# Kernel tuning notes

Measured on AMD Instinct MI355X. Metric: run time of the kernel, lower is better.

Reference implementation:

```python
import jax, jax.numpy as jnp
import numpy as np

OBS_DIM, ACT_DIM, LATENT_DIM, BELIEF_DIM, T = 128, 32, 512, 1024, 32768


def setup_inputs() -> dict:
    key = jax.random.key(0)
    ks = jax.random.split(key, 8)
    s_ih = 1.0 / np.sqrt(BELIEF_DIM)
    s_enc = 1.0 / np.sqrt(OBS_DIM)
    return {
        "obs_seq": jax.random.normal(ks[0], (T, OBS_DIM), jnp.float32),
        "act_seq": jax.random.normal(ks[1], (T, ACT_DIM), jnp.float32),
        "enc_w": jax.random.uniform(ks[2], (LATENT_DIM, OBS_DIM), jnp.float32, -s_enc, s_enc),
        "enc_b": jax.random.uniform(ks[3], (LATENT_DIM,), jnp.float32, -s_enc, s_enc),
        "w_ih": jax.random.uniform(ks[4], (3 * BELIEF_DIM, LATENT_DIM + ACT_DIM), jnp.float32, -s_ih, s_ih),
        "w_hh": jax.random.uniform(ks[5], (3 * BELIEF_DIM, BELIEF_DIM), jnp.float32, -s_ih, s_ih),
        "b_ih": jax.random.uniform(ks[6], (3 * BELIEF_DIM,), jnp.float32, -s_ih, s_ih),
        "b_hh": jax.random.uniform(ks[7], (3 * BELIEF_DIM,), jnp.float32, -s_ih, s_ih),
    }


def reference(obs_seq, act_seq, enc_w, enc_b, w_ih, w_hh, b_ih, b_hh):
    H = w_hh.shape[1]
    # Encoder over all timesteps at once: (T, latent)
    z_seq = jnp.tanh(obs_seq @ enc_w.T + enc_b)
    # a_prev[t] = act_seq[t-1], zeros at t=0
    a_prev = jnp.concatenate(
        [jnp.zeros((1, act_seq.shape[1]), act_seq.dtype), act_seq[:-1]], axis=0)
    x_seq = jnp.concatenate([z_seq, a_prev], axis=-1)  # (T, latent+act)
    # Precompute input-side gate projections as one big GEMM: (T, 3H)
    gi_seq = x_seq @ w_ih.T + b_ih

    def step(h, gi_t):
        gh = w_hh @ h + b_hh  # (3H,)
        ir, iz, inn = jnp.split(gi_t, 3)
        hr, hz, hn = jnp.split(gh, 3)
        r = jax.nn.sigmoid(ir + hr)
        z = jax.nn.sigmoid(iz + hz)
        n = jnp.tanh(inn + r * hn)
        h_new = (1.0 - z) * n + z * h
        return h_new, h_new

    h0 = jnp.zeros((H,), x_seq.dtype)
    _, beliefs = jax.lax.scan(step, h0, gi_seq)
    return beliefs  # (T, belief_dim)
```

## Files before the change

kernel.cpp:

```cpp
#include <hip/hip_runtime.h>
#include <stdint.h>

#define T_STEPS 32768
#define HDIM    1024
#define LDIM    512
#define ADIM    32
#define NWG     128
#define NOUT    8

__global__ __launch_bounds__(256) void encoder_kernel(
    const float* __restrict__ obs,
    const float* __restrict__ w,
    const float* __restrict__ b,
    float* __restrict__ z)
{
    __shared__ float As[64][65];
    __shared__ float Bs[64][65];

    const int tile_n = blockIdx.x;
    const int tile_t = blockIdx.y;
    const int tid = threadIdx.x;
    const int ty = tid >> 4;
    const int tx = tid & 15;

    float acc[4][4] = {};

    for (int kt = 0; kt < 2; ++kt) {
        #pragma unroll
        for (int it = 0; it < 4; ++it) {
            int lin = it * 1024 + tid * 4;
            int r = lin >> 6, c = lin & 63;
            float4 va = *(const float4*)&obs[(size_t)(tile_t * 64 + r) * 128 + kt * 64 + c];
            As[r][c] = va.x; As[r][c+1] = va.y; As[r][c+2] = va.z; As[r][c+3] = va.w;
            float4 vb = *(const float4*)&w[(size_t)(tile_n * 64 + r) * 128 + kt * 64 + c];
            Bs[r][c] = vb.x; Bs[r][c+1] = vb.y; Bs[r][c+2] = vb.z; Bs[r][c+3] = vb.w;
        }
        __syncthreads();

        for (int k = 0; k < 64; ++k) {
            float av[4], bv[4];
            #pragma unroll
            for (int a = 0; a < 4; ++a) av[a] = As[ty * 4 + a][k];
            #pragma unroll
            for (int c = 0; c < 4; ++c) bv[c] = Bs[tx * 4 + c][k];
            #pragma unroll
            for (int a = 0; a < 4; ++a)
                #pragma unroll
                for (int c = 0; c < 4; ++c)
                    acc[a][c] = fmaf(av[a], bv[c], acc[a][c]);
        }
        __syncthreads();
    }

    #pragma unroll
    for (int a = 0; a < 4; ++a) {
        int row = tile_t * 64 + ty * 4 + a;
        #pragma unroll
        for (int c = 0; c < 4; ++c) {
            int col = tile_n * 64 + tx * 4 + c;
            z[(size_t)row * LDIM + col] = tanhf(acc[a][c] + b[col]);
        }
    }
}

__global__ __launch_bounds__(256, 1) void gru_kernel(
    float* __restrict__ out,
    const float* __restrict__ z_seq,
    const float* __restrict__ act,
    const float* __restrict__ w_ih,
    const float* __restrict__ w_hh,
    const float* __restrict__ b_ih,
    const float* __restrict__ b_hh,
    uint64_t* __restrict__ hbuf)
{
    __shared__ float h_lds[HDIM];
    __shared__ float z_lds[LDIM];
    __shared__ float a_lds[ADIM];

    const int tid  = threadIdx.x;
    const int wg   = blockIdx.x;
    const int grp  = tid >> 5;
    const int lane = tid & 31;
    const int i    = wg * NOUT + grp;

    float whr[32], whz[32], whn[32];
    {
        const float* pr = &w_hh[(size_t)i * HDIM + lane];
        const float* pz = &w_hh[(size_t)(HDIM + i) * HDIM + lane];
        const float* pn = &w_hh[(size_t)(2 * HDIM + i) * HDIM + lane];
        #pragma unroll
        for (int j = 0; j < 32; ++j) {
            whr[j] = pr[32 * j]; whz[j] = pz[32 * j]; whn[j] = pn[32 * j];
        }
    }
    float wir[17], wiz[17], win[17];
    {
        const float* pr = &w_ih[(size_t)i * 544 + lane];
        const float* pz = &w_ih[(size_t)(HDIM + i) * 544 + lane];
        const float* pn = &w_ih[(size_t)(2 * HDIM + i) * 544 + lane];
        #pragma unroll
        for (int j = 0; j < 17; ++j) {
            wir[j] = pr[32 * j]; wiz[j] = pz[32 * j]; win[j] = pn[32 * j];
        }
    }
    #pragma unroll
    for (int j = 0; j < 32; ++j) {
        asm volatile("" : "+v"(whr[j]), "+v"(whz[j]), "+v"(whn[j]));
    }
    #pragma unroll
    for (int j = 0; j < 17; ++j) {
        asm volatile("" : "+v"(wir[j]), "+v"(wiz[j]), "+v"(win[j]));
    }

    const float bir  = b_ih[i], biz = b_ih[HDIM + i], bin_ = b_ih[2 * HDIM + i];
    const float bhr  = b_hh[i], bhz = b_hh[HDIM + i], bhn  = b_hh[2 * HDIM + i];

    for (int q = tid; q < HDIM; q += 256) h_lds[q] = 0.0f;
    __syncthreads();

    for (int t = 0; t < T_STEPS; ++t) {
        if (tid < 128) {
            float4 v = *(const float4*)&z_seq[(size_t)t * LDIM + tid * 4];
            *(float4*)&z_lds[tid * 4] = v;
        } else if (tid < 160) {
            int q = tid - 128;
            a_lds[q] = (t == 0) ? 0.0f : act[(size_t)(t - 1) * ADIM + q];
        }

        if (t > 0) {
            const uint64_t* bp = hbuf + ((size_t)((t - 1) & 1)) * HDIM + tid * 4;
            const uint32_t want = (uint32_t)t;
            uint64_t v[4];
            int done = 0;
            while (done != 0xF) {
                #pragma unroll
                for (int q = 0; q < 4; ++q) {
                    if (!(done & (1 << q))) {
                        v[q] = __hip_atomic_load(bp + q, __ATOMIC_RELAXED,
                                                 __HIP_MEMORY_SCOPE_AGENT);
                    }
                }
                #pragma unroll
                for (int q = 0; q < 4; ++q) {
                    if (!(done & (1 << q)) && (uint32_t)(v[q] >> 32) == want)
                        done |= (1 << q);
                }
            }
            float4 hv;
            hv.x = __uint_as_float((uint32_t)v[0]);
            hv.y = __uint_as_float((uint32_t)v[1]);
            hv.z = __uint_as_float((uint32_t)v[2]);
            hv.w = __uint_as_float((uint32_t)v[3]);
            *(float4*)&h_lds[tid * 4] = hv;
        }
        __syncthreads();

        float sr = 0.f, sz = 0.f, sn = 0.f;
        #pragma unroll
        for (int j = 0; j < 32; ++j) {
            float hv = h_lds[lane + 32 * j];
            sr = fmaf(whr[j], hv, sr);
            sz = fmaf(whz[j], hv, sz);
            sn = fmaf(whn[j], hv, sn);
        }
        float gr = 0.f, gz = 0.f, gn = 0.f;
        #pragma unroll
        for (int j = 0; j < 16; ++j) {
            float xv = z_lds[lane + 32 * j];
            gr = fmaf(wir[j], xv, gr);
            gz = fmaf(wiz[j], xv, gz);
            gn = fmaf(win[j], xv, gn);
        }
        {
            float xa = a_lds[lane];
            gr = fmaf(wir[16], xa, gr);
            gz = fmaf(wiz[16], xa, gz);
            gn = fmaf(win[16], xa, gn);
        }

        float vr = sr + gr, vz = sz + gz;
        #pragma unroll
        for (int m = 16; m >= 1; m >>= 1) {
            vr += __shfl_xor(vr, m);
            vz += __shfl_xor(vz, m);
            sn += __shfl_xor(sn, m);
            gn += __shfl_xor(gn, m);
        }

        if (lane == 0) {
            float r  = 1.0f / (1.0f + expf(-(vr + bir + bhr)));
            float zg = 1.0f / (1.0f + expf(-(vz + biz + bhz)));
            float n  = tanhf(gn + bin_ + r * (sn + bhn));
            float hold = h_lds[i];
            float hnew = (1.0f - zg) * n + zg * hold;
            uint64_t pk = ((uint64_t)(uint32_t)(t + 1) << 32) |
                          (uint64_t)__float_as_uint(hnew);
            __hip_atomic_store(&hbuf[((size_t)(t & 1)) * HDIM + i], pk,
                               __ATOMIC_RELAXED, __HIP_MEMORY_SCOPE_AGENT);
            out[(size_t)t * HDIM + i] = hnew;
        }
        __syncthreads();
    }
}

extern "C" void kernel_launch(void* const* d_in, const int* in_sizes, int n_in,
                              void* d_out, int out_size, void* d_ws, size_t ws_size,
                              hipStream_t stream) {
    const float* obs   = (const float*)d_in[0];
    const float* act   = (const float*)d_in[1];
    const float* enc_w = (const float*)d_in[2];
    const float* enc_b = (const float*)d_in[3];
    const float* w_ih  = (const float*)d_in[4];
    const float* w_hh  = (const float*)d_in[5];
    const float* b_ih  = (const float*)d_in[6];
    const float* b_hh  = (const float*)d_in[7];
    float* out = (float*)d_out;

    uint64_t* hbuf  = (uint64_t*)d_ws;
    float*    z_seq = (float*)((char*)d_ws + 65536);

    hipMemsetAsync(hbuf, 0, 2 * HDIM * sizeof(uint64_t), stream);

    encoder_kernel<<<dim3(8, 512), 256, 0, stream>>>(obs, enc_w, enc_b, z_seq);

    void* args[] = {(void*)&out, (void*)&z_seq, (void*)&act, (void*)&w_ih,
                    (void*)&w_hh, (void*)&b_ih, (void*)&b_hh, (void*)&hbuf};
    hipLaunchCooperativeKernel((void*)gru_kernel, dim3(NWG), dim3(256),
                               args, 0, stream);
}
```

Measured before the change: 100.3 ms.

## Split h polling from input loads and publish hidden state from one wave

The per-step cross-workgroup handoff is reorganised. Threads 128-255 now poll the previous hidden state, eight packed entries each, while threads 0-127 load the encoder latent and action for the step, so the polling runs alongside the input fetch. The new hidden values are first gathered in a small shared array, then one wave issues the eight flag-tagged atomic stores and a vectorized write of the output row. This cuts scattered stores per step on the serial critical path, at the cost of an extra barrier before publishing and fewer threads doing the polling.

```diff
diff --git a/kernel.cpp b/kernel.cpp
--- a/kernel.cpp
+++ b/kernel.cpp
@@ -76,6 +76,7 @@
     __shared__ float h_lds[HDIM];
     __shared__ float z_lds[LDIM];
     __shared__ float a_lds[ADIM];
+    __shared__ float h_pub[NOUT];
 
     const int tid  = threadIdx.x;
     const int wg   = blockIdx.x;
@@ -122,36 +123,40 @@
         if (tid < 128) {
             float4 v = *(const float4*)&z_seq[(size_t)t * LDIM + tid * 4];
             *(float4*)&z_lds[tid * 4] = v;
-        } else if (tid < 160) {
-            int q = tid - 128;
-            a_lds[q] = (t == 0) ? 0.0f : act[(size_t)(t - 1) * ADIM + q];
-        }
-
-        if (t > 0) {
-            const uint64_t* bp = hbuf + ((size_t)((t - 1) & 1)) * HDIM + tid * 4;
+            if (tid < ADIM) {
+                a_lds[tid] = (t == 0) ? 0.0f : act[(size_t)(t - 1) * ADIM + tid];
+            }
+        } else if (t > 0) {
+            const int q = tid - 128;
+            const uint64_t* bp = hbuf + ((size_t)((t - 1) & 1)) * HDIM + q * 8;
             const uint32_t want = (uint32_t)t;
-            uint64_t v[4];
+            uint64_t v[8];
             int done = 0;
-            while (done != 0xF) {
+            while (done != 0xFF) {
                 #pragma unroll
-                for (int q = 0; q < 4; ++q) {
-                    if (!(done & (1 << q))) {
-                        v[q] = __hip_atomic_load(bp + q, __ATOMIC_RELAXED,
+                for (int k = 0; k < 8; ++k) {
+                    if (!(done & (1 << k))) {
+                        v[k] = __hip_atomic_load(bp + k, __ATOMIC_RELAXED,
                                                  __HIP_MEMORY_SCOPE_AGENT);
                     }
                 }
                 #pragma unroll
-                for (int q = 0; q < 4; ++q) {
-                    if (!(done & (1 << q)) && (uint32_t)(v[q] >> 32) == want)
-                        done |= (1 << q);
+                for (int k = 0; k < 8; ++k) {
+                    if (!(done & (1 << k)) && (uint32_t)(v[k] >> 32) == want)
+                        done |= (1 << k);
                 }
             }
-            float4 hv;
-            hv.x = __uint_as_float((uint32_t)v[0]);
-            hv.y = __uint_as_float((uint32_t)v[1]);
-            hv.z = __uint_as_float((uint32_t)v[2]);
-            hv.w = __uint_as_float((uint32_t)v[3]);
-            *(float4*)&h_lds[tid * 4] = hv;
+            float4 h0, h1;
+            h0.x = __uint_as_float((uint32_t)v[0]);
+            h0.y = __uint_as_float((uint32_t)v[1]);
+            h0.z = __uint_as_float((uint32_t)v[2]);
+            h0.w = __uint_as_float((uint32_t)v[3]);
+            h1.x = __uint_as_float((uint32_t)v[4]);
+            h1.y = __uint_as_float((uint32_t)v[5]);
+            h1.z = __uint_as_float((uint32_t)v[6]);
+            h1.w = __uint_as_float((uint32_t)v[7]);
+            *(float4*)&h_lds[q * 8]     = h0;
+            *(float4*)&h_lds[q * 8 + 4] = h1;
         }
         __syncthreads();
 
@@ -192,14 +197,21 @@
             float zg = 1.0f / (1.0f + expf(-(vz + biz + bhz)));
             float n  = tanhf(gn + bin_ + r * (sn + bhn));
             float hold = h_lds[i];
-            float hnew = (1.0f - zg) * n + zg * hold;
+            h_pub[grp] = (1.0f - zg) * n + zg * hold;
+        }
+        __syncthreads();
+
+        if (tid < NOUT) {
             uint64_t pk = ((uint64_t)(uint32_t)(t + 1) << 32) |
-                          (uint64_t)__float_as_uint(hnew);
-            __hip_atomic_store(&hbuf[((size_t)(t & 1)) * HDIM + i], pk,
-                               __ATOMIC_RELAXED, __HIP_MEMORY_SCOPE_AGENT);
-            out[(size_t)t * HDIM + i] = hnew;
-        }
-        __syncthreads();
+                          (uint64_t)__float_as_uint(h_pub[tid]);
+            __hip_atomic_store(&hbuf[((size_t)(t & 1)) * HDIM + wg * NOUT + tid],
+                               pk, __ATOMIC_RELAXED, __HIP_MEMORY_SCOPE_AGENT);
+        } else if (tid == NOUT) {
+            float4 o0 = *(const float4*)&h_pub[0];
+            float4 o1 = *(const float4*)&h_pub[4];
+            *(float4*)&out[(size_t)t * HDIM + wg * NOUT]     = o0;
+            *(float4*)&out[(size_t)t * HDIM + wg * NOUT + 4] = o1;
+        }
     }
 }
 
```

Result: faster. 94.40 ms (-5.9%).

## Restructure GRU recurrence to single-wavefront workgroups with register-resident hidden state

Applied to the files above, without the earlier changes.

The recurrent kernel moves from 128 workgroups of 256 threads to 256 single-wavefront workgroups, each computing 4 hidden units. Each lane polls the flagged hidden-state buffer straight into registers and reduces with wave-wide shuffles, which drops the LDS staging and both per-step __syncthreads barriers. The hbuf layout is padded to 8 slots per workgroup, and sigmoid/tanh use fast exp/rcp intrinsics. The launch switches from a cooperative launch to a plain one, so the spin-wait relies on all 256 workgroups being co-resident without a guarantee, and the fast math is slightly less accurate.

```diff
diff --git a/kernel.cpp b/kernel.cpp
--- a/kernel.cpp
+++ b/kernel.cpp
@@ -5,8 +5,17 @@
 #define HDIM    1024
 #define LDIM    512
 #define ADIM    32
-#define NWG     128
-#define NOUT    8
+#define NWG     256
+#define NOUT    4
+
+__device__ __forceinline__ float fast_sigmoid(float x) {
+    float e = __expf(-x);
+    return __builtin_amdgcn_rcpf(1.0f + e);
+}
+__device__ __forceinline__ float fast_tanh(float x) {
+    float e = __expf(2.0f * x);
+    return 1.0f - 2.0f * __builtin_amdgcn_rcpf(1.0f + e);
+}
 
 __global__ __launch_bounds__(256) void encoder_kernel(
     const float* __restrict__ obs,
@@ -63,7 +72,7 @@
     }
 }
 
-__global__ __launch_bounds__(256, 1) void gru_kernel(
+__global__ __launch_bounds__(64, 1) void gru_kernel(
     float* __restrict__ out,
     const float* __restrict__ z_seq,
     const float* __restrict__ act,
@@ -73,133 +82,162 @@
     const float* __restrict__ b_hh,
     uint64_t* __restrict__ hbuf)
 {
-    __shared__ float h_lds[HDIM];
-    __shared__ float z_lds[LDIM];
-    __shared__ float a_lds[ADIM];
-
-    const int tid  = threadIdx.x;
-    const int wg   = blockIdx.x;
-    const int grp  = tid >> 5;
-    const int lane = tid & 31;
-    const int i    = wg * NOUT + grp;
-
-    float whr[32], whz[32], whn[32];
-    {
-        const float* pr = &w_hh[(size_t)i * HDIM + lane];
-        const float* pz = &w_hh[(size_t)(HDIM + i) * HDIM + lane];
-        const float* pn = &w_hh[(size_t)(2 * HDIM + i) * HDIM + lane];
-        #pragma unroll
-        for (int j = 0; j < 32; ++j) {
-            whr[j] = pr[32 * j]; whz[j] = pz[32 * j]; whn[j] = pn[32 * j];
-        }
-    }
-    float wir[17], wiz[17], win[17];
-    {
-        const float* pr = &w_ih[(size_t)i * 544 + lane];
-        const float* pz = &w_ih[(size_t)(HDIM + i) * 544 + lane];
-        const float* pn = &w_ih[(size_t)(2 * HDIM + i) * 544 + lane];
-        #pragma unroll
-        for (int j = 0; j < 17; ++j) {
-            wir[j] = pr[32 * j]; wiz[j] = pz[32 * j]; win[j] = pn[32 * j];
-        }
-    }
-    #pragma unroll
-    for (int j = 0; j < 32; ++j) {
-        asm volatile("" : "+v"(whr[j]), "+v"(whz[j]), "+v"(whn[j]));
-    }
-    #pragma unroll
-    for (int j = 0; j < 17; ++j) {
-        asm volatile("" : "+v"(wir[j]), "+v"(wiz[j]), "+v"(win[j]));
-    }
-
-    const float bir  = b_ih[i], biz = b_ih[HDIM + i], bin_ = b_ih[2 * HDIM + i];
-    const float bhr  = b_hh[i], bhz = b_hh[HDIM + i], bhn  = b_hh[2 * HDIM + i];
-
-    for (int q = tid; q < HDIM; q += 256) h_lds[q] = 0.0f;
-    __syncthreads();
+    const int lane  = threadIdx.x;
+    const int wg    = blockIdx.x;
+    const int obase = wg * NOUT;
+
+    float whh[3][4][4][4];
+    #pragma unroll
+    for (int g = 0; g < 3; ++g)
+        #pragma unroll
+        for (int o = 0; o < 4; ++o) {
+            const float* row = &w_hh[(size_t)(g * HDIM + obase + o) * HDIM];
+            #pragma unroll
+            for (int m = 0; m < 4; ++m)
+                #pragma unroll
+                for (int c = 0; c < 4; ++c)
+                    whh[g][o][m][c] = row[m * 256 + lane * 4 + c];
+        }
+    float wz[3][4][8];
+    #pragma unroll
+    for (int g = 0; g < 3; ++g)
+        #pragma unroll
+        for (int o = 0; o < 4; ++o) {
+            const float* row = &w_ih[(size_t)(g * HDIM + obase + o) * 544];
+            #pragma unroll
+            for (int j = 0; j < 8; ++j)
+                wz[g][o][j] = row[lane * 8 + j];
+        }
+    float wa[3][4];
+    #pragma unroll
+    for (int g = 0; g < 3; ++g)
+        #pragma unroll
+        for (int o = 0; o < 4; ++o)
+            wa[g][o] = (lane < ADIM)
+                ? w_ih[(size_t)(g * HDIM + obase + o) * 544 + LDIM + lane] : 0.0f;
+
+    #pragma unroll
+    for (int g = 0; g < 3; ++g)
+        #pragma unroll
+        for (int o = 0; o < 4; ++o) {
+            #pragma unroll
+            for (int m = 0; m < 4; ++m)
+                #pragma unroll
+                for (int c = 0; c < 4; ++c)
+                    asm volatile("" : "+v"(whh[g][o][m][c]));
+            #pragma unroll
+            for (int j = 0; j < 8; ++j)
+                asm volatile("" : "+v"(wz[g][o][j]));
+            asm volatile("" : "+v"(wa[g][o]));
+        }
+
+    const int oc  = lane & 3;
+    const int myo = obase + oc;
+    const float bias_r = b_ih[myo] + b_hh[myo];
+    const float bias_z = b_ih[HDIM + myo] + b_hh[HDIM + myo];
+    const float bin_   = b_ih[2 * HDIM + myo];
+    const float bhn    = b_hh[2 * HDIM + myo];
+
+    float hold = 0.0f;
 
     for (int t = 0; t < T_STEPS; ++t) {
-        if (tid < 128) {
-            float4 v = *(const float4*)&z_seq[(size_t)t * LDIM + tid * 4];
-            *(float4*)&z_lds[tid * 4] = v;
-        } else if (tid < 160) {
-            int q = tid - 128;
-            a_lds[q] = (t == 0) ? 0.0f : act[(size_t)(t - 1) * ADIM + q];
-        }
-
-        if (t > 0) {
-            const uint64_t* bp = hbuf + ((size_t)((t - 1) & 1)) * HDIM + tid * 4;
+        float4 z0 = *(const float4*)&z_seq[(size_t)t * LDIM + lane * 8];
+        float4 z1 = *(const float4*)&z_seq[(size_t)t * LDIM + lane * 8 + 4];
+        float av = 0.0f;
+        if (t > 0 && lane < ADIM) av = act[(size_t)(t - 1) * ADIM + lane];
+
+        float h[4][4];
+        if (t == 0) {
+            #pragma unroll
+            for (int m = 0; m < 4; ++m)
+                #pragma unroll
+                for (int c = 0; c < 4; ++c) h[m][c] = 0.0f;
+        } else {
+            const uint64_t* bp = hbuf + ((size_t)((t - 1) & 1)) * (NWG * 8);
             const uint32_t want = (uint32_t)t;
-            uint64_t v[4];
+            uint64_t v[4][4];
             int done = 0;
             while (done != 0xF) {
                 #pragma unroll
-                for (int q = 0; q < 4; ++q) {
-                    if (!(done & (1 << q))) {
-                        v[q] = __hip_atomic_load(bp + q, __ATOMIC_RELAXED,
-                                                 __HIP_MEMORY_SCOPE_AGENT);
+                for (int m = 0; m < 4; ++m) {
+                    if (!(done & (1 << m))) {
+                        const uint64_t* lp = bp + (size_t)(m * 64 + lane) * 8;
+                        #pragma unroll
+                        for (int c = 0; c < 4; ++c)
+                            v[m][c] = __hip_atomic_load(lp + c, __ATOMIC_RELAXED,
+                                                        __HIP_MEMORY_SCOPE_AGENT);
                     }
                 }
                 #pragma unroll
-                for (int q = 0; q < 4; ++q) {
-                    if (!(done & (1 << q)) && (uint32_t)(v[q] >> 32) == want)
-                        done |= (1 << q);
+                for (int m = 0; m < 4; ++m) {
+                    if (!(done & (1 << m))) {
+                        bool ok = true;
+                        #pragma unroll
+                        for (int c = 0; c < 4; ++c)
+                            ok = ok && ((uint32_t)(v[m][c] >> 32) == want);
+                        if (ok) done |= (1 << m);
+                    }
                 }
             }
-            float4 hv;
-            hv.x = __uint_as_float((uint32_t)v[0]);
-            hv.y = __uint_as_float((uint32_t)v[1]);
-            hv.z = __uint_as_float((uint32_t)v[2]);
-            hv.w = __uint_as_float((uint32_t)v[3]);
-            *(float4*)&h_lds[tid * 4] = hv;
-        }
-        __syncthreads();
-
-        float sr = 0.f, sz = 0.f, sn = 0.f;
-        #pragma unroll
-        for (int j = 0; j < 32; ++j) {
-            float hv = h_lds[lane + 32 * j];
-            sr = fmaf(whr[j], hv, sr);
-            sz = fmaf(whz[j], hv, sz);
-            sn = fmaf(whn[j], hv, sn);
-        }
-        float gr = 0.f, gz = 0.f, gn = 0.f;
-        #pragma unroll
-        for (int j = 0; j < 16; ++j) {
-            float xv = z_lds[lane + 32 * j];
-            gr = fmaf(wir[j], xv, gr);
-            gz = fmaf(wiz[j], xv, gz);
-            gn = fmaf(win[j], xv, gn);
-        }
-        {
-            float xa = a_lds[lane];
-            gr = fmaf(wir[16], xa, gr);
-            gz = fmaf(wiz[16], xa, gz);
-            gn = fmaf(win[16], xa, gn);
-        }
-
-        float vr = sr + gr, vz = sz + gz;
-        #pragma unroll
-        for (int m = 16; m >= 1; m >>= 1) {
-            vr += __shfl_xor(vr, m);
-            vz += __shfl_xor(vz, m);
-            sn += __shfl_xor(sn, m);
-            gn += __shfl_xor(gn, m);
-        }
-
-        if (lane == 0) {
-            float r  = 1.0f / (1.0f + expf(-(vr + bir + bhr)));
-            float zg = 1.0f / (1.0f + expf(-(vz + biz + bhz)));
-            float n  = tanhf(gn + bin_ + r * (sn + bhn));
-            float hold = h_lds[i];
-            float hnew = (1.0f - zg) * n + zg * hold;
+            #pragma unroll
+            for (int m = 0; m < 4; ++m)
+                #pragma unroll
+                for (int c = 0; c < 4; ++c)
+                    h[m][c] = __uint_as_float((uint32_t)v[m][c]);
+        }
+
+        float ar[4] = {}, az[4] = {}, anh[4] = {}, ani[4] = {};
+        float zv[8] = {z0.x, z0.y, z0.z, z0.w, z1.x, z1.y, z1.z, z1.w};
+        #pragma unroll
+        for (int o = 0; o < 4; ++o) {
+            #pragma unroll
+            for (int m = 0; m < 4; ++m)
+                #pragma unroll
+                for (int c = 0; c < 4; ++c) {
+                    float hv = h[m][c];
+                    ar[o]  = fmaf(whh[0][o][m][c], hv, ar[o]);
+                    az[o]  = fmaf(whh[1][o][m][c], hv, az[o]);
+                    anh[o] = fmaf(whh[2][o][m][c], hv, anh[o]);
+                }
+            #pragma unroll
+            for (int j = 0; j < 8; ++j) {
+                ar[o]  = fmaf(wz[0][o][j], zv[j], ar[o]);
+                az[o]  = fmaf(wz[1][o][j], zv[j], az[o]);
+                ani[o] = fmaf(wz[2][o][j], zv[j], ani[o]);
+            }
+            ar[o]  = fmaf(wa[0][o], av, ar[o]);
+            az[o]  = fmaf(wa[1][o], av, az[o]);
+            ani[o] = fmaf(wa[2][o], av, ani[o]);
+        }
+
+        #pragma unroll
+        for (int o = 0; o < 4; ++o) {
+            #pragma unroll
+            for (int m = 1; m <= 32; m <<= 1) {
+                ar[o]  += __shfl_xor(ar[o],  m);
+                az[o]  += __shfl_xor(az[o],  m);
+                anh[o] += __shfl_xor(anh[o], m);
+                ani[o] += __shfl_xor(ani[o], m);
+            }
+        }
+        float s_r  = (oc == 0) ? ar[0]  : (oc == 1) ? ar[1]  : (oc == 2) ? ar[2]  : ar[3];
+        float s_z  = (oc == 0) ? az[0]  : (oc == 1) ? az[1]  : (oc == 2) ? az[2]  : az[3];
+        float s_nh = (oc == 0) ? anh[0] : (oc == 1) ? anh[1] : (oc == 2) ? anh[2] : anh[3];
+        float s_ni = (oc == 0) ? ani[0] : (oc == 1) ? ani[1] : (oc == 2) ? ani[2] : ani[3];
+
+        float r    = fast_sigmoid(s_r + bias_r);
+        float zg   = fast_sigmoid(s_z + bias_z);
+        float n    = fast_tanh(s_ni + bin_ + r * (s_nh + bhn));
+        float hnew = (1.0f - zg) * n + zg * hold;
+        hold = hnew;
+
+        if (lane < 4) {
             uint64_t pk = ((uint64_t)(uint32_t)(t + 1) << 32) |
                           (uint64_t)__float_as_uint(hnew);
-            __hip_atomic_store(&hbuf[((size_t)(t & 1)) * HDIM + i], pk,
-                               __ATOMIC_RELAXED, __HIP_MEMORY_SCOPE_AGENT);
-            out[(size_t)t * HDIM + i] = hnew;
-        }
-        __syncthreads();
+            __hip_atomic_store(&hbuf[((size_t)(t & 1)) * (NWG * 8) + wg * 8 + lane],
+                               pk, __ATOMIC_RELAXED, __HIP_MEMORY_SCOPE_AGENT);
+            out[(size_t)t * HDIM + obase + lane] = hnew;
+        }
     }
 }
 
@@ -219,12 +257,10 @@
     uint64_t* hbuf  = (uint64_t*)d_ws;
     float*    z_seq = (float*)((char*)d_ws + 65536);
 
-    hipMemsetAsync(hbuf, 0, 2 * HDIM * sizeof(uint64_t), stream);
+    hipMemsetAsync(hbuf, 0, 2 * NWG * 8 * sizeof(uint64_t), stream);
 
     encoder_kernel<<<dim3(8, 512), 256, 0, stream>>>(obs, enc_w, enc_b, z_seq);
 
-    void* args[] = {(void*)&out, (void*)&z_seq, (void*)&act, (void*)&w_ih,
-                    (void*)&w_hh, (void*)&b_ih, (void*)&b_hh, (void*)&hbuf};
-    hipLaunchCooperativeKernel((void*)gru_kernel, dim3(NWG), dim3(256),
-                               args, 0, stream);
-}
+    gru_kernel<<<dim3(NWG), dim3(64), 0, stream>>>(
+        out, z_seq, act, w_ih, w_hh, b_ih, b_hh, hbuf);
+}
```

After: 170.4 ms. 1.7x slower.
